# Performance work log

Hardware: AMD Instinct MI355X
Metric: run time of the kernel (lower is better)

## Reference

```python
import jax, jax.numpy as jnp
import numpy as np

HIDDEN = 1024
HEADS = 16
HEAD_DIM = HIDDEN // HEADS  # 64
ROPE_DIM = 64
ROPE_BASE = 10000.0
B, T = 2, 2048


def setup_inputs() -> dict:
    key = jax.random.key(0)
    k1, k2, k3, k4, k5, k6 = jax.random.split(key, 6)
    x = jax.random.normal(k1, (B, T, HIDDEN), dtype=jnp.float32)
    input_ids = jax.random.randint(k2, (B, T), 0, 32000)
    # torch Linear weights: [out_features, in_features]
    qkv_w = jax.random.normal(k3, (3 * HIDDEN, HIDDEN), dtype=jnp.float32) * (1.0 / np.sqrt(HIDDEN))
    qkv_b = jnp.zeros((3 * HIDDEN,), dtype=jnp.float32)
    out_w = jax.random.normal(k4, (HIDDEN, HIDDEN), dtype=jnp.float32) * (1.0 / np.sqrt(HIDDEN))
    out_b = jnp.zeros((HIDDEN,), dtype=jnp.float32)
    global_idx = jnp.array([0, 1, 2], dtype=jnp.int64)  # special_tokens values
    return {"x": x, "input_ids": input_ids, "qkv_w": qkv_w, "qkv_b": qkv_b,
            "out_w": out_w, "out_b": out_b, "global_idx": global_idx}


def _rope_cos_sin(t, offset=0):
    inv_freq = 1.0 / (ROPE_BASE ** (jnp.arange(0, ROPE_DIM, 2, dtype=jnp.float32) / ROPE_DIM))  # [ROPE_DIM/2]
    pos = jnp.arange(offset, offset + t, dtype=jnp.float32)
    freqs = pos[:, None] * inv_freq[None, :]  # [T, ROPE_DIM/2]
    return jnp.cos(freqs)[None, None], jnp.sin(freqs)[None, None]  # [1,1,T,ROPE_DIM/2]


def _apply_rotary(x, cos, sin):
    x_rot, x_pass = x[..., :ROPE_DIM], x[..., ROPE_DIM:]
    half = ROPE_DIM // 2
    x1, x2 = x_rot[..., :half], x_rot[..., half:]
    return jnp.concatenate([x1 * cos - x2 * sin, x1 * sin + x2 * cos, x_pass], axis=-1)


def reference(x, input_ids, qkv_w, qkv_b, out_w, out_b, global_idx):
    b, t, _ = x.shape
    qkv = x @ qkv_w.T + qkv_b  # [B,T,3*HIDDEN]
    q, k, v = jnp.split(qkv, 3, axis=-1)
    # -> [B, H, T, Dh]
    reshape = lambda z: z.reshape(b, t, HEADS, HEAD_DIM).transpose(0, 2, 1, 3)
    q, k, v = reshape(q), reshape(k), reshape(v)
    cos, sin = _rope_cos_sin(t)
    q = _apply_rotary(q, cos, sin)
    k = _apply_rotary(k, cos, sin)
    # causal + global-query mask
    causal = jnp.tril(jnp.ones((t, t), dtype=bool))[None, None]  # [1,1,T,T]
    global_mask = jnp.isin(input_ids, global_idx)  # [B,T]
    allow = causal | global_mask[:, None, :, None]  # [B,1,T,T]
    scale = jnp.sqrt(jnp.float32(HEAD_DIM))
    logits = jnp.einsum('bhqd,bhkd->bhqk', q, k) / scale
    neg = -jnp.finfo(logits.dtype).max
    logits = jnp.where(allow, logits, neg)
    attn = jax.nn.softmax(logits, axis=-1)
    out = jnp.einsum('bhqk,bhkd->bhqd', attn, v)  # [B,H,T,Dh]
    out = out.transpose(0, 2, 1, 3).reshape(b, t, HEADS * HEAD_DIM)
    return out @ out_w.T + out_b
```

## Files before the change

kernel.cpp:

```cpp
#include <hip/hip_runtime.h>
#include <hip/hip_bf16.h>
#include <math.h>

typedef __bf16 bf16;
typedef __bf16 bf16x4 __attribute__((ext_vector_type(4)));
typedef __bf16 bf16x8 __attribute__((ext_vector_type(8)));
typedef float floatx4 __attribute__((ext_vector_type(4)));

#define HIDDEN 1024
#define NHEADS 16
#define HDIM 64
#define TSEQ 2048
#define NBATCH 2
#define MTOT (NBATCH * TSEQ)

__device__ inline void glds16(bf16* lds, const bf16* g)
{
  __builtin_amdgcn_global_load_lds(
      (const __attribute__((address_space(1))) unsigned int*)g,
      (__attribute__((address_space(3))) unsigned int*)lds, 16, 0, 0);
}

__global__ __launch_bounds__(256) void prep_kernel(
    const float* __restrict__ x, bf16* __restrict__ xb,
    const float* __restrict__ qkv_w, bf16* __restrict__ qkv_wb,
    float2* __restrict__ rope)
{
  const int bid = blockIdx.x;
  if (bid >= 3584) {
    const int e0 = ((bid - 3584) * 256 + threadIdx.x) * 4;
    const int t = e0 >> 5;
    const int d2 = e0 & 31;
#pragma unroll
    for (int j = 0; j < 4; j++) {
      const float inv = exp2f((float)(d2 + j) * -0.41524100f);
      float s, c;
      sincosf((float)t * inv, &s, &c);
      rope[e0 + j] = make_float2(c, s);
    }
    return;
  }
  const float* src = (bid < 2048) ? x : qkv_w;
  bf16* dst = (bid < 2048) ? xb : qkv_wb;
  const int i = (((bid < 2048) ? bid : bid - 2048) * 256 + threadIdx.x) * 8;
  const floatx4 u = *(const floatx4*)(src + i);
  const floatx4 v = *(const floatx4*)(src + i + 4);
  bf16x8 r;
#pragma unroll
  for (int j = 0; j < 4; j++) { r[j] = (bf16)u[j]; r[4 + j] = (bf16)v[j]; }
  *(bf16x8*)(dst + i) = r;
}

__global__ __launch_bounds__(256) void cvt_f32_bf16(
    const float* __restrict__ src, bf16* __restrict__ dst, int n)
{
  const int i = (blockIdx.x * 256 + threadIdx.x) * 8;
  if (i >= n) return;
  const floatx4 u = *(const floatx4*)(src + i);
  const floatx4 v = *(const floatx4*)(src + i + 4);
  bf16x8 r;
#pragma unroll
  for (int j = 0; j < 4; j++) { r[j] = (bf16)u[j]; r[4 + j] = (bf16)v[j]; }
  *(bf16x8*)(dst + i) = r;
}


#define STAGE(buf, kk)                                                      \
  glds16(&As[buf][(wv * 32) * 32], ga0 + (kk));                             \
  glds16(&As[buf][(wv * 32 + 16) * 32], ga0 + (size_t)16 * K + (kk));       \
  glds16(&Bs[buf][(wv * 32) * 32], gb0 + (kk));                             \
  glds16(&Bs[buf][(wv * 32 + 16) * 32], gb0 + (size_t)16 * K + (kk));

#define COMPUTE(buf)                                                        \
  {                                                                         \
    bf16x8 af[4], bfr[4];                                                   \
    _Pragma("unroll") for (int i = 0; i < 4; i++)                           \
        af[i] = *(const bf16x8*)(&As[buf][(wm + i * 16 + l16) * 32 + qsw]); \
    _Pragma("unroll") for (int j = 0; j < 4; j++)                           \
        bfr[j] = *(const bf16x8*)(&Bs[buf][(wn + j * 16 + l16) * 32 + qsw]);\
    _Pragma("unroll") for (int i = 0; i < 4; i++)                           \
        _Pragma("unroll") for (int j = 0; j < 4; j++)                       \
            acc[i][j] = __builtin_amdgcn_mfma_f32_16x16x32_bf16(            \
                af[i], bfr[j], acc[i][j], 0, 0, 0);                         \
  }

__global__ __launch_bounds__(256) void gemm_qkv(
    const bf16* __restrict__ A, const bf16* __restrict__ W,
    const float* __restrict__ bias, const float2* __restrict__ rope,
    bf16* __restrict__ Qb, bf16* __restrict__ Kb, bf16* __restrict__ Vt,
    int M, int N, int K)
{
  __shared__ bf16 As[3][128 * 32];
  __shared__ bf16 Bs[3][128 * 32];

  const int tid  = threadIdx.x;
  const int lane = tid & 63;
  const int wv   = tid >> 6;
  const int quad = lane >> 4;
  const int l16  = lane & 15;

  const int f   = blockIdx.x;
  const int xcd = f & 7;
  const int rr  = f >> 3;
  const int bx  = (xcd & 1) * 12 + (rr % 12);
  const int by  = (xcd >> 1) * 8 + (rr / 12);
  const int m0 = by * 128;
  const int n0 = bx * 128;

  const int wm = (wv >> 1) * 64;
  const int wn = (wv & 1) * 64;
  const int srow = lane >> 2;
  const int scol = ((lane & 3) ^ ((lane >> 3) & 3)) * 8;
  const int qsw  = (quad ^ ((l16 >> 1) & 3)) * 8;

  const bf16* ga0 = A + (size_t)(m0 + wv * 32 + srow) * K + scol;
  const bf16* gb0 = W + (size_t)(n0 + wv * 32 + srow) * K + scol;

  floatx4 acc[4][4];
#pragma unroll
  for (int i = 0; i < 4; i++)
#pragma unroll
    for (int j = 0; j < 4; j++) acc[i][j] = (floatx4){0.f, 0.f, 0.f, 0.f};

  STAGE(0, 0);
  STAGE(1, 32);
  int cur = 0;
  const int nsteps = K / 32;
#pragma unroll 1
  for (int t = 0; t < nsteps - 1; t++) {
    asm volatile("s_waitcnt vmcnt(4)" ::: "memory");
    __builtin_amdgcn_s_barrier();
    if (t + 2 < nsteps) {
      const int nb = (cur >= 1) ? cur - 1 : cur + 2;
      STAGE(nb, (t + 2) * 32);
    }
    COMPUTE(cur);
    cur = (cur == 2) ? 0 : cur + 1;
  }
  asm volatile("s_waitcnt vmcnt(0)" ::: "memory");
  __builtin_amdgcn_s_barrier();
  COMPUTE(cur);

  const int sect = n0 >> 10;
  const int hw   = ((n0 & 1023) + wn) >> 6;

  float bs[4];
#pragma unroll
  for (int j = 0; j < 4; j++) bs[j] = bias[n0 + wn + j * 16 + l16];

  if (sect < 2) {
    bf16* dst = sect ? Kb : Qb;
#pragma unroll
    for (int i = 0; i < 4; i++) {
      const int gmBase = m0 + wm + i * 16 + quad * 4;
#pragma unroll
      for (int r = 0; r < 4; r++) {
        const int gm = gmBase + r;
        const int b_ = gm >> 11, t = gm & 2047;
        const size_t rowbase = ((size_t)(b_ * NHEADS + hw) * TSEQ + t) * HDIM;
        const float2 cs0 = rope[t * 32 + l16];
        const float2 cs1 = rope[t * 32 + 16 + l16];
        const float x1a = acc[i][0][r] + bs[0];
        const float x2a = acc[i][2][r] + bs[2];
        const float x1b = acc[i][1][r] + bs[1];
        const float x2b = acc[i][3][r] + bs[3];
        dst[rowbase + l16]      = (bf16)(x1a * cs0.x - x2a * cs0.y);
        dst[rowbase + 32 + l16] = (bf16)(x1a * cs0.y + x2a * cs0.x);
        dst[rowbase + 16 + l16] = (bf16)(x1b * cs1.x - x2b * cs1.y);
        dst[rowbase + 48 + l16] = (bf16)(x1b * cs1.y + x2b * cs1.x);
      }
    }
  } else {
#pragma unroll
    for (int j = 0; j < 4; j++) {
      const int d = j * 16 + l16;
#pragma unroll
      for (int i = 0; i < 4; i++) {
        const int gmBase = m0 + wm + i * 16 + quad * 4;
        const int b_ = gmBase >> 11, t0 = gmBase & 2047;
        bf16x4 vv;
#pragma unroll
        for (int r = 0; r < 4; r++) vv[r] = (bf16)(acc[i][j][r] + bs[j]);
        *(bf16x4*)(Vt + ((size_t)((b_ * NHEADS + hw) * HDIM + d)) * TSEQ + t0) = vv;
      }
    }
  }
}

__global__ __launch_bounds__(256) void gemm_out(
    const bf16* __restrict__ A, const bf16* __restrict__ W,
    const float* __restrict__ bias, float* __restrict__ C,
    int M, int N, int K)
{
  __shared__ bf16 As[3][128 * 32];
  __shared__ bf16 Bs[3][64 * 32];

  const int tid  = threadIdx.x;
  const int lane = tid & 63;
  const int wv   = tid >> 6;
  const int quad = lane >> 4;
  const int l16  = lane & 15;

  const int f   = blockIdx.x;
  const int xcd = f & 7;
  const int rr  = f >> 3;
  const int bx  = (xcd & 1) * 8 + (rr & 7);
  const int by  = (xcd >> 1) * 8 + (rr >> 3);
  const int m0 = by * 128;
  const int n0 = bx * 64;
  const int wm = wv * 32;

  const int srow = lane >> 2;
  const int scol = ((lane & 3) ^ ((lane >> 3) & 3)) * 8;
  const int qsw  = (quad ^ ((l16 >> 1) & 3)) * 8;

  const bf16* ga0 = A + (size_t)(m0 + wv * 32 + srow) * K + scol;
  const bf16* gb0 = W + (size_t)(n0 + wv * 16 + srow) * K + scol;

  floatx4 acc[2][4];
#pragma unroll
  for (int i = 0; i < 2; i++)
#pragma unroll
    for (int j = 0; j < 4; j++) acc[i][j] = (floatx4){0.f, 0.f, 0.f, 0.f};

#define STAGE_O(buf, kk)                                                    \
  glds16(&As[buf][(wv * 32) * 32], ga0 + (kk));                             \
  glds16(&As[buf][(wv * 32 + 16) * 32], ga0 + (size_t)16 * K + (kk));       \
  glds16(&Bs[buf][(wv * 16) * 32], gb0 + (kk));

#define COMPUTE_O(buf)                                                      \
  {                                                                         \
    bf16x8 af[2], bfr[4];                                                   \
    _Pragma("unroll") for (int i = 0; i < 2; i++)                           \
        af[i] = *(const bf16x8*)(&As[buf][(wm + i * 16 + l16) * 32 + qsw]); \
    _Pragma("unroll") for (int j = 0; j < 4; j++)                           \
        bfr[j] = *(const bf16x8*)(&Bs[buf][(j * 16 + l16) * 32 + qsw]);     \
    _Pragma("unroll") for (int i = 0; i < 2; i++)                           \
        _Pragma("unroll") for (int j = 0; j < 4; j++)                       \
            acc[i][j] = __builtin_amdgcn_mfma_f32_16x16x32_bf16(            \
                af[i], bfr[j], acc[i][j], 0, 0, 0);                         \
  }

  STAGE_O(0, 0);
  STAGE_O(1, 32);
  int cur = 0;
  const int nsteps = K / 32;
#pragma unroll 1
  for (int t = 0; t < nsteps - 1; t++) {
    asm volatile("s_waitcnt vmcnt(3)" ::: "memory");
    __builtin_amdgcn_s_barrier();
    if (t + 2 < nsteps) {
      const int nb = (cur >= 1) ? cur - 1 : cur + 2;
      STAGE_O(nb, (t + 2) * 32);
    }
    COMPUTE_O(cur);
    cur = (cur == 2) ? 0 : cur + 1;
  }
  asm volatile("s_waitcnt vmcnt(0)" ::: "memory");
  __builtin_amdgcn_s_barrier();
  COMPUTE_O(cur);

#pragma unroll
  for (int i = 0; i < 2; i++) {
    const int gmBase = m0 + wm + i * 16 + quad * 4;
#pragma unroll
    for (int j = 0; j < 4; j++) {
      const int gn = n0 + j * 16 + l16;
      const float bsv = bias[gn];
#pragma unroll
      for (int r = 0; r < 4; r++)
        C[(size_t)(gmBase + r) * N + gn] = acc[i][j][r] + bsv;
    }
  }
}

__device__ inline int swz(int g) { return (g & ~7) | ((g ^ (g >> 3) ^ (g >> 6)) & 7); }

__global__ __launch_bounds__(256) void attn_kernel(
    const bf16* __restrict__ Q, const bf16* __restrict__ K,
    const bf16* __restrict__ Vt, bf16* __restrict__ O,
    const int* __restrict__ ids, const int* __restrict__ gidx)
{
  __shared__ bf16 Ks[4096];
  __shared__ bf16 Vs[4096];
  __shared__ int flags[4];

  const int tid  = threadIdx.x;
  const int lane = tid & 63;
  const int wv   = tid >> 6;
  const int quad = lane >> 4;
  const int l16  = lane & 15;

  const int xcd = blockIdx.x & 7;
  const int j   = blockIdx.x >> 3;
  const int bh  = xcd * 4 + (j >> 4);
  const int p   = j & 15;
  const int b  = bh >> 4;
  const int h  = bh & 15;

  const bf16* Qp = Q + (size_t)bh * TSEQ * HDIM;
  const bf16* Kp = K + (size_t)bh * TSEQ * HDIM;
  const bf16* Vp = Vt + (size_t)bh * HDIM * TSEQ;

  const int rK  = tid >> 3;
  const int dcK = tid & 7;
  const int gk = ((rK >> 2) & 1) * 128 + (dcK >> 2) * 64 +
                 ((dcK & 3) * 16 + (((rK >> 3) << 2) | (rK & 3)));
  const int kd0 = swz(gk) * 8, kd1 = swz(gk + 256) * 8;
  const int dV = tid >> 3;
  const int uV = tid & 7;
  const int gv = (uV >> 2) * 256 + (dV >> 4) * 64 + ((uV & 3) * 16 + (dV & 15));
  const int vd0 = swz(gv) * 8, vd1 = swz(gv + 128) * 8;

  const int g0v = gidx[0], g1v = gidx[1], g2v = gidx[2];

#pragma unroll
  for (int ph = 0; ph < 2; ph++) {
    const int qt = ph ? p : (31 - p);
    const int q0 = qt * 64 + wv * 16;

    const bf16x8 qf0 = *(const bf16x8*)(Qp + (size_t)(q0 + l16) * HDIM + quad * 8);
    const bf16x8 qf1 = *(const bf16x8*)(Qp + (size_t)(q0 + l16) * HDIM + 32 + quad * 8);

    const int myq = q0 + l16;
    const int myid = ids[b * TSEQ + myq];
    const int gl = (myid == g0v) | (myid == g1v) | (myid == g2v);
    flags[wv] = __any(gl);
    __syncthreads();
    const int anyg = flags[0] | flags[1] | flags[2] | flags[3];
    const int kmax = anyg ? TSEQ : (qt * 64 + 64);

    float lsum = 0.f;
    floatx4 o[4];
#pragma unroll
    for (int nt = 0; nt < 4; nt++) o[nt] = (floatx4){0.f, 0.f, 0.f, 0.f};

    bf16x8 kA = *(const bf16x8*)(Kp + tid * 8);
    bf16x8 kB = *(const bf16x8*)(Kp + 2048 + tid * 8);
    bf16x8 vA = *(const bf16x8*)(Vp + (size_t)dV * TSEQ + uV * 8);
    bf16x8 vB = *(const bf16x8*)(Vp + (size_t)(dV + 32) * TSEQ + uV * 8);

    for (int k0 = 0; k0 < kmax; k0 += 64) {
      __syncthreads();
      *(bf16x8*)(Ks + kd0) = kA;
      *(bf16x8*)(Ks + kd1) = kB;
      *(bf16x8*)(Vs + vd0) = vA;
      *(bf16x8*)(Vs + vd1) = vB;
      __syncthreads();

      if (k0 + 64 < kmax) {
        const bf16* kc = Kp + (size_t)(k0 + 64) * HDIM;
        kA = *(const bf16x8*)(kc + tid * 8);
        kB = *(const bf16x8*)(kc + 2048 + tid * 8);
        vA = *(const bf16x8*)(Vp + (size_t)dV * TSEQ + k0 + 64 + uV * 8);
        vB = *(const bf16x8*)(Vp + (size_t)(dV + 32) * TSEQ + k0 + 64 + uV * 8);
      }

#pragma unroll
      for (int g = 0; g < 2; g++) {
        const int kb = k0 + g * 32;
        const int rb = g * 256 + lane;
        const bf16x8 a00 = *(const bf16x8*)(Ks + swz(rb) * 8);
        const bf16x8 a01 = *(const bf16x8*)(Ks + swz(rb + 64) * 8);
        const bf16x8 a10 = *(const bf16x8*)(Ks + swz(rb + 128) * 8);
        const bf16x8 a11 = *(const bf16x8*)(Ks + swz(rb + 192) * 8);
        floatx4 s0 = (floatx4){0.f, 0.f, 0.f, 0.f};
        floatx4 s1 = (floatx4){0.f, 0.f, 0.f, 0.f};
        s0 = __builtin_amdgcn_mfma_f32_16x16x32_bf16(a00, qf0, s0, 0, 0, 0);
        s0 = __builtin_amdgcn_mfma_f32_16x16x32_bf16(a01, qf1, s0, 0, 0, 0);
        s1 = __builtin_amdgcn_mfma_f32_16x16x32_bf16(a10, qf0, s1, 0, 0, 0);
        s1 = __builtin_amdgcn_mfma_f32_16x16x32_bf16(a11, qf1, s1, 0, 0, 0);

        bf16x8 pf;
#pragma unroll
        for (int r = 0; r < 4; r++) {
          const int key0 = kb + quad * 8 + r;
          const int key1 = key0 + 4;
          const float p0 = (gl || key0 <= myq) ? __expf(s0[r] * 0.125f) : 0.f;
          const float p1 = (gl || key1 <= myq) ? __expf(s1[r] * 0.125f) : 0.f;
          lsum += p0 + p1;
          pf[r]     = (bf16)p0;
          pf[4 + r] = (bf16)p1;
        }

#pragma unroll
        for (int nt = 0; nt < 4; nt++) {
          const bf16x8 vf = *(const bf16x8*)(Vs + swz(g * 256 + nt * 64 + lane) * 8);
          o[nt] = __builtin_amdgcn_mfma_f32_16x16x32_bf16(pf, vf, o[nt], 0, 0, 0);
        }
      }
    }

    lsum += __shfl_xor(lsum, 16);
    lsum += __shfl_xor(lsum, 32);

#pragma unroll
    for (int r = 0; r < 4; r++) {
      const float inv = 1.0f / __shfl(lsum, quad * 4 + r);
      const int q = q0 + quad * 4 + r;
      const size_t rowoff = ((size_t)b * TSEQ + q) * HIDDEN + h * HDIM;
#pragma unroll
      for (int nt = 0; nt < 4; nt++)
        O[rowoff + nt * 16 + l16] = (bf16)(o[nt][r] * inv);
    }
  }
}

extern "C" void kernel_launch(void* const* d_in, const int* in_sizes, int n_in,
                              void* d_out, int out_size, void* d_ws, size_t ws_size,
                              hipStream_t stream)
{
  const float* x     = (const float*)d_in[0];
  const int*   ids   = (const int*)d_in[1];
  const float* qkv_w = (const float*)d_in[2];
  const float* qkv_b = (const float*)d_in[3];
  const float* out_w = (const float*)d_in[4];
  const float* out_b = (const float*)d_in[5];
  const int*   gidx  = (const int*)d_in[6];
  float* out = (float*)d_out;

  char* ws = (char*)d_ws;
  bf16* Q      = (bf16*)(ws);
  bf16* Kb     = (bf16*)(ws + (size_t)(8u << 20));
  bf16* Vt     = (bf16*)(ws + (size_t)(16u << 20));
  bf16* slot24 = (bf16*)(ws + (size_t)(24u << 20));
  bf16* xb     = slot24;
  bf16* O      = slot24;
  bf16* out_wb = (bf16*)(ws + (size_t)(16u << 20));
  bf16* qkv_wb = (bf16*)d_out;
  float2* rope = (float2*)((char*)d_out + (size_t)(6u << 20));

  prep_kernel<<<3648, 256, 0, stream>>>(x, xb, qkv_w, qkv_wb, rope);
  gemm_qkv<<<768, 256, 0, stream>>>(
      xb, qkv_wb, qkv_b, rope, Q, Kb, Vt, MTOT, 3 * HIDDEN, HIDDEN);
  attn_kernel<<<512, 256, 0, stream>>>(Q, Kb, Vt, O, ids, gidx);
  cvt_f32_bf16<<<512, 256, 0, stream>>>(out_w, out_wb, HIDDEN * HIDDEN);
  gemm_out<<<512, 256, 0, stream>>>(
      O, out_wb, out_b, out, MTOT, HIDDEN, HIDDEN);
}
```

Baseline: 198.7 us.

## Enlarge QKV GEMM to 256x256 tiles with 8 waves and phased pipelining

The QKV projection GEMM moves from 128x128 tiles with 4 waves to 256x256 tiles with 8 waves per block. It uses double-buffered 64-wide K stages split into four half-phases that interleave LDS reads, async global-to-LDS loads and MFMA, with s_setprio raised around the MFMA bursts. The aim is more data reuse per loaded byte and better overlap of loads with math. The cost is only 192 blocks on a 256-CU part, so some CUs sit idle, plus higher register and LDS pressure (128 KB of LDS).

```diff
diff --git a/kernel.cpp b/kernel.cpp
--- a/kernel.cpp
+++ b/kernel.cpp
@@ -64,82 +64,105 @@
   *(bf16x8*)(dst + i) = r;
 }
 
-
-#define STAGE(buf, kk)                                                      \
-  glds16(&As[buf][(wv * 32) * 32], ga0 + (kk));                             \
-  glds16(&As[buf][(wv * 32 + 16) * 32], ga0 + (size_t)16 * K + (kk));       \
-  glds16(&Bs[buf][(wv * 32) * 32], gb0 + (kk));                             \
-  glds16(&Bs[buf][(wv * 32 + 16) * 32], gb0 + (size_t)16 * K + (kk));
-
-#define COMPUTE(buf)                                                        \
-  {                                                                         \
-    bf16x8 af[4], bfr[4];                                                   \
-    _Pragma("unroll") for (int i = 0; i < 4; i++)                           \
-        af[i] = *(const bf16x8*)(&As[buf][(wm + i * 16 + l16) * 32 + qsw]); \
-    _Pragma("unroll") for (int j = 0; j < 4; j++)                           \
-        bfr[j] = *(const bf16x8*)(&Bs[buf][(wn + j * 16 + l16) * 32 + qsw]);\
-    _Pragma("unroll") for (int i = 0; i < 4; i++)                           \
-        _Pragma("unroll") for (int j = 0; j < 4; j++)                       \
-            acc[i][j] = __builtin_amdgcn_mfma_f32_16x16x32_bf16(            \
-                af[i], bfr[j], acc[i][j], 0, 0, 0);                         \
-  }
-
-__global__ __launch_bounds__(256) void gemm_qkv(
+__global__ __launch_bounds__(512, 2) void gemm_qkv(
     const bf16* __restrict__ A, const bf16* __restrict__ W,
     const float* __restrict__ bias, const float2* __restrict__ rope,
     bf16* __restrict__ Qb, bf16* __restrict__ Kb, bf16* __restrict__ Vt,
     int M, int N, int K)
 {
-  __shared__ bf16 As[3][128 * 32];
-  __shared__ bf16 Bs[3][128 * 32];
+  __shared__ bf16 As[2][2][256 * 32];
+  __shared__ bf16 Bs[2][2][256 * 32];
 
   const int tid  = threadIdx.x;
   const int lane = tid & 63;
   const int wv   = tid >> 6;
   const int quad = lane >> 4;
   const int l16  = lane & 15;
+  const int wm   = (wv >> 2) * 128;
+  const int wn   = (wv & 3) * 64;
 
   const int f   = blockIdx.x;
   const int xcd = f & 7;
   const int rr  = f >> 3;
-  const int bx  = (xcd & 1) * 12 + (rr % 12);
-  const int by  = (xcd >> 1) * 8 + (rr / 12);
-  const int m0 = by * 128;
-  const int n0 = bx * 128;
-
-  const int wm = (wv >> 1) * 64;
-  const int wn = (wv & 1) * 64;
+  const int bx  = (xcd & 1) * 6 + rr % 6;
+  const int by  = (xcd >> 1) * 4 + rr / 6;
+  const int m0 = by * 256;
+  const int n0 = bx * 256;
+
   const int srow = lane >> 2;
   const int scol = ((lane & 3) ^ ((lane >> 3) & 3)) * 8;
   const int qsw  = (quad ^ ((l16 >> 1) & 3)) * 8;
 
-  const bf16* ga0 = A + (size_t)(m0 + wv * 32 + srow) * K + scol;
-  const bf16* gb0 = W + (size_t)(n0 + wv * 32 + srow) * K + scol;
-
-  floatx4 acc[4][4];
-#pragma unroll
-  for (int i = 0; i < 4; i++)
+  const bf16* gaBase = A + (size_t)(m0 + wv * 16 + srow) * K + scol;
+  const bf16* gbBase = W + (size_t)(n0 + wv * 16 + srow) * K + scol;
+  const int ldst = wv * 512 + lane * 8;
+
+#define STG_A(d, kh, kcol)                                                   \
+  glds16(&As[d][kh][ldst],        gaBase + (kcol));                          \
+  glds16(&As[d][kh][ldst + 4096], gaBase + (size_t)128 * K + (kcol));
+#define STG_B(d, kh, kcol)                                                   \
+  glds16(&Bs[d][kh][ldst],        gbBase + (kcol));                          \
+  glds16(&Bs[d][kh][ldst + 4096], gbBase + (size_t)128 * K + (kcol));
+
+#define RD_PH(d, kh, mh)                                                     \
+  _Pragma("unroll") for (int i = 0; i < 4; i++)                              \
+    af[i] = *(const bf16x8*)(&As[d][kh][(wm + (mh) * 64 + i * 16 + l16) * 32 + qsw]); \
+  _Pragma("unroll") for (int j = 0; j < 4; j++)                              \
+    bfr[j] = *(const bf16x8*)(&Bs[d][kh][(wn + j * 16 + l16) * 32 + qsw]);
+
+#define MM_PH(mh)                                                            \
+  _Pragma("unroll") for (int i = 0; i < 4; i++)                              \
+    _Pragma("unroll") for (int j = 0; j < 4; j++)                            \
+      acc[(mh) * 4 + i][j] = __builtin_amdgcn_mfma_f32_16x16x32_bf16(        \
+          af[i], bfr[j], acc[(mh) * 4 + i][j], 0, 0, 0);
+
+  floatx4 acc[8][4];
+#pragma unroll
+  for (int i = 0; i < 8; i++)
 #pragma unroll
     for (int j = 0; j < 4; j++) acc[i][j] = (floatx4){0.f, 0.f, 0.f, 0.f};
 
-  STAGE(0, 0);
-  STAGE(1, 32);
-  int cur = 0;
-  const int nsteps = K / 32;
+  STG_A(0, 0, 0); STG_B(0, 0, 0);
+  STG_A(0, 1, 32); STG_B(0, 1, 32);
+  asm volatile("s_waitcnt vmcnt(4)" ::: "memory");
+  __builtin_amdgcn_s_barrier();
+
+  const int nt = K >> 6;
 #pragma unroll 1
-  for (int t = 0; t < nsteps - 1; t++) {
-    asm volatile("s_waitcnt vmcnt(4)" ::: "memory");
+  for (int t = 0; t < nt; t++) {
+    const int c = t & 1;
+    const int kn = (t + 1) * 64;
+    const bool more = (t + 1 < nt);
+    bf16x8 af[4], bfr[4];
+
+    RD_PH(c, 0, 0);
+    if (more) { STG_A(c ^ 1, 0, kn); }
     __builtin_amdgcn_s_barrier();
-    if (t + 2 < nsteps) {
-      const int nb = (cur >= 1) ? cur - 1 : cur + 2;
-      STAGE(nb, (t + 2) * 32);
-    }
-    COMPUTE(cur);
-    cur = (cur == 2) ? 0 : cur + 1;
-  }
-  asm volatile("s_waitcnt vmcnt(0)" ::: "memory");
-  __builtin_amdgcn_s_barrier();
-  COMPUTE(cur);
+    __builtin_amdgcn_s_setprio(1); MM_PH(0); __builtin_amdgcn_s_setprio(0);
+
+    RD_PH(c, 0, 1);
+    if (more) {
+      STG_B(c ^ 1, 0, kn);
+      asm volatile("s_waitcnt vmcnt(4)" ::: "memory");
+    } else {
+      asm volatile("s_waitcnt vmcnt(0)" ::: "memory");
+    }
+    __builtin_amdgcn_s_barrier();
+    __builtin_amdgcn_s_setprio(1); MM_PH(1); __builtin_amdgcn_s_setprio(0);
+
+    RD_PH(c, 1, 0);
+    if (more) { STG_A(c ^ 1, 1, kn + 32); }
+    __builtin_amdgcn_s_barrier();
+    __builtin_amdgcn_s_setprio(1); MM_PH(0); __builtin_amdgcn_s_setprio(0);
+
+    RD_PH(c, 1, 1);
+    if (more) {
+      STG_B(c ^ 1, 1, kn + 32);
+      asm volatile("s_waitcnt vmcnt(4)" ::: "memory");
+    }
+    __builtin_amdgcn_s_barrier();
+    __builtin_amdgcn_s_setprio(1); MM_PH(1); __builtin_amdgcn_s_setprio(0);
+  }
 
   const int sect = n0 >> 10;
   const int hw   = ((n0 & 1023) + wn) >> 6;
@@ -151,7 +174,7 @@
   if (sect < 2) {
     bf16* dst = sect ? Kb : Qb;
 #pragma unroll
-    for (int i = 0; i < 4; i++) {
+    for (int i = 0; i < 8; i++) {
       const int gmBase = m0 + wm + i * 16 + quad * 4;
 #pragma unroll
       for (int r = 0; r < 4; r++) {
@@ -175,7 +198,7 @@
     for (int j = 0; j < 4; j++) {
       const int d = j * 16 + l16;
 #pragma unroll
-      for (int i = 0; i < 4; i++) {
+      for (int i = 0; i < 8; i++) {
         const int gmBase = m0 + wm + i * 16 + quad * 4;
         const int b_ = gmBase >> 11, t0 = gmBase & 2047;
         bf16x4 vv;
@@ -192,8 +215,8 @@
     const float* __restrict__ bias, float* __restrict__ C,
     int M, int N, int K)
 {
-  __shared__ bf16 As[3][128 * 32];
-  __shared__ bf16 Bs[3][64 * 32];
+  __shared__ bf16 As2[3][128 * 32];
+  __shared__ bf16 Bs2[3][64 * 32];
 
   const int tid  = threadIdx.x;
   const int lane = tid & 63;
@@ -224,17 +247,17 @@
     for (int j = 0; j < 4; j++) acc[i][j] = (floatx4){0.f, 0.f, 0.f, 0.f};
 
 #define STAGE_O(buf, kk)                                                    \
-  glds16(&As[buf][(wv * 32) * 32], ga0 + (kk));                             \
-  glds16(&As[buf][(wv * 32 + 16) * 32], ga0 + (size_t)16 * K + (kk));       \
-  glds16(&Bs[buf][(wv * 16) * 32], gb0 + (kk));
+  glds16(&As2[buf][(wv * 32) * 32], ga0 + (kk));                            \
+  glds16(&As2[buf][(wv * 32 + 16) * 32], ga0 + (size_t)16 * K + (kk));      \
+  glds16(&Bs2[buf][(wv * 16) * 32], gb0 + (kk));
 
 #define COMPUTE_O(buf)                                                      \
   {                                                                         \
     bf16x8 af[2], bfr[4];                                                   \
     _Pragma("unroll") for (int i = 0; i < 2; i++)                           \
-        af[i] = *(const bf16x8*)(&As[buf][(wm + i * 16 + l16) * 32 + qsw]); \
+        af[i] = *(const bf16x8*)(&As2[buf][(wm + i * 16 + l16) * 32 + qsw]);\
     _Pragma("unroll") for (int j = 0; j < 4; j++)                           \
-        bfr[j] = *(const bf16x8*)(&Bs[buf][(j * 16 + l16) * 32 + qsw]);     \
+        bfr[j] = *(const bf16x8*)(&Bs2[buf][(j * 16 + l16) * 32 + qsw]);    \
     _Pragma("unroll") for (int i = 0; i < 2; i++)                           \
         _Pragma("unroll") for (int j = 0; j < 4; j++)                       \
             acc[i][j] = __builtin_amdgcn_mfma_f32_16x16x32_bf16(            \
@@ -431,7 +454,7 @@
   float2* rope = (float2*)((char*)d_out + (size_t)(6u << 20));
 
   prep_kernel<<<3648, 256, 0, stream>>>(x, xb, qkv_w, qkv_wb, rope);
-  gemm_qkv<<<768, 256, 0, stream>>>(
+  gemm_qkv<<<192, 512, 0, stream>>>(
       xb, qkv_wb, qkv_b, rope, Q, Kb, Vt, MTOT, 3 * HIDDEN, HIDDEN);
   attn_kernel<<<512, 256, 0, stream>>>(Q, Kb, Vt, O, ids, gidx);
   cvt_f32_bf16<<<512, 256, 0, stream>>>(out_w, out_wb, HIDDEN * HIDDEN);
```

Measured after the change: 189.4 us. 4.7% less time.
